# Performance work log

Measured on AMD Instinct MI355X. Metric: run time of the kernel, lower is better.

Reference implementation:

```python
import jax, jax.numpy as jnp
import numpy as np

B, C_IN, T, DIM_H, HEADS, K = 64, 64, 512, 64, 2, 9
N = B * T            # graph nodes = batch * cycle_size
E = 524288           # edges (avg degree 16)
D = HEADS * DIM_H    # 128, GATv2 concat output
EPS = 1e-5
SLOPE = 0.2          # GATv2 leaky_relu negative slope


def setup_inputs() -> dict:
    key = jax.random.key(0)
    ks = jax.random.split(key, 12)
    s = 0.05
    return {
        'x': jax.random.normal(ks[0], (B, C_IN, T), jnp.float32),
        'edge_index': jax.random.randint(ks[1], (2, E), 0, N, jnp.int32),
        'bn0_g': jnp.ones((C_IN,), jnp.float32),
        'bn0_b': jnp.zeros((C_IN,), jnp.float32),
        'W_l': jax.random.normal(ks[2], (C_IN, D), jnp.float32) * s,
        'W_r': jax.random.normal(ks[3], (C_IN, D), jnp.float32) * s,
        'att': jax.random.normal(ks[4], (HEADS, DIM_H), jnp.float32) * s,
        'gat_b': jnp.zeros((D,), jnp.float32),
        'bn1_g': jnp.ones((D,), jnp.float32),
        'bn1_b': jnp.zeros((D,), jnp.float32),
        'conv_w': jax.random.normal(ks[5], (T, T, K), jnp.float32) * s,
        'conv_b': jnp.zeros((T,), jnp.float32),
        'bn2_g': jnp.ones((T,), jnp.float32),
        'bn2_b': jnp.zeros((T,), jnp.float32),
    }


def _bn(x, g, b, axes, shape):
    # BatchNorm1d in training mode: biased batch stats per channel
    m = jnp.mean(x, axes, keepdims=True)
    v = jnp.var(x, axes, keepdims=True)
    return (x - m) * jax.lax.rsqrt(v + EPS) * g.reshape(shape) + b.reshape(shape)


def _gatv2(x, edge_index, W_l, W_r, att, bias):
    # PyG GATv2Conv: out_i = sum_j softmax_j(att . leaky_relu(xl_j + xr_i)) * xl_j
    xl = (x @ W_l).reshape(N, HEADS, DIM_H)
    xr = (x @ W_r).reshape(N, HEADS, DIM_H)
    loops = jnp.arange(N, dtype=edge_index.dtype)  # add_self_loops=True
    src = jnp.concatenate([edge_index[0], loops])
    dst = jnp.concatenate([edge_index[1], loops])
    h = xl[src] + xr[dst]                       # [E+N, H, dh]
    h = jnp.where(h > 0, h, SLOPE * h)
    logits = jnp.einsum('ehd,hd->eh', h, att)   # [E+N, H]
    mmax = jax.ops.segment_max(logits, dst, num_segments=N)
    a = jnp.exp(logits - mmax[dst])
    z = jax.ops.segment_sum(a, dst, num_segments=N)
    alpha = a / z[dst]                          # scatter-softmax over incoming edges
    out = jax.ops.segment_sum(alpha[:, :, None] * xl[src], dst, num_segments=N)
    return out.reshape(N, D) + bias


def reference(x, edge_index, bn0_g, bn0_b, W_l, W_r, att, gat_b,
              bn1_g, bn1_b, conv_w, conv_b, bn2_g, bn2_b):
    # b0 (batch_size > 1), x: [B, C_IN, T]
    x = _bn(x, bn0_g, bn0_b, (0, 2), (1, C_IN, 1))
    # (skip_connection branch is dead code: its result is overwritten)
    # torch .view on contiguous [B,C,T] -> [B*T, C] == raw reshape
    xn = x.reshape(N, C_IN)
    xn = jax.nn.relu(_bn(_gatv2(xn, edge_index, W_l, W_r, att, gat_b),
                         bn1_g, bn1_b, (0,), (1, D)))
    x3 = xn.reshape(B, D, T)
    residual = x3
    xt = jnp.transpose(x3, (0, 2, 1))           # [B, T, D]: channels=T, length=D
    y = jax.lax.conv_general_dilated(xt, conv_w, (1,), 'SAME',
                                     dimension_numbers=('NCH', 'OIH', 'NCH'))
    y = y + conv_b[None, :, None]
    y = jax.nn.relu(_bn(y, bn2_g, bn2_b, (0, 2), (1, T, 1)))
    y = jnp.transpose(y, (0, 2, 1))             # [B, D, T]
    # dropout(p=0.1) is identity in eval
    return residual + y
```

## Files before the change

### kernel.cpp

```cpp
#include <hip/hip_runtime.h>
#include <stdint.h>

typedef __attribute__((ext_vector_type(8))) __bf16 bf16x8;
typedef __attribute__((ext_vector_type(4))) float f32x4;

#define DEVI __device__ __forceinline__

constexpr int Bn = 64, CIN = 64, Tn = 512, Nn = 32768, Dn = 128;
constexpr int En = 524288, ENn = En + Nn;
constexpr float EPSf = 1e-5f;

constexpr size_t OFF_XL   = 0;
constexpr size_t OFF_XR   = 8388608;
constexpr size_t OFF_GPAD = 16777216;
constexpr size_t OFF_WRE  = 25690112;
constexpr size_t OFF_WT   = 30408704;
constexpr size_t OFF_CNT  = 30441472;
constexpr size_t OFF_OFFS = 30572544;
constexpr size_t OFF_CUR  = 30703632;
constexpr size_t OFF_SRC  = 30834704;
constexpr size_t OFF_STAT = 33062928;
constexpr size_t OFF_SUM0 = OFF_STAT;
constexpr size_t OFF_SQ0  = OFF_STAT + 256;
constexpr size_t OFF_SUM1 = OFF_STAT + 512;
constexpr size_t OFF_SQ1  = OFF_STAT + 1024;
constexpr size_t OFF_SC0  = OFF_STAT + 1536;
constexpr size_t OFF_SH0  = OFF_STAT + 1792;
constexpr size_t OFF_SC1  = OFF_STAT + 2048;
constexpr size_t OFF_SH1  = OFF_STAT + 2560;
constexpr size_t OFF_SC2  = OFF_STAT + 3072;
constexpr size_t OFF_SH2  = OFF_STAT + 5120;
constexpr size_t WS_NEED  = OFF_STAT + 7168;

DEVI float bf2f(unsigned short u){
  union { unsigned int u; float f; } x; x.u = ((unsigned int)u) << 16; return x.f;
}
DEVI unsigned short f2bf(float f){
  union { float f; unsigned int u; } x; x.f = f;
  unsigned int lsb = (x.u >> 16) & 1u;
  return (unsigned short)((x.u + 0x7fffu + lsb) >> 16);
}
DEVI void gl_lds16(const void* g, void* l){
  __builtin_amdgcn_global_load_lds(
      (const __attribute__((address_space(1))) unsigned int*)g,
      (__attribute__((address_space(3))) unsigned int*)l, 16, 0, 0);
}
DEVI bool finitef(float v){ return (v == v) && (fabsf(v) < 1e30f); }
DEVI float red32(float p){
  p += __shfl_xor(p, 1);  p += __shfl_xor(p, 2);  p += __shfl_xor(p, 4);
  p += __shfl_xor(p, 8);  p += __shfl_xor(p, 16);
  return p;
}
DEVI size_t gpad_addr(int b, int m, int d){
  int ig = m >> 2;
  int chunk = ((m & 3) << 1) | (d >> 6);
  int est = ((d & 63) + ((ig & 7) << 3)) & 63;
  return (size_t)b * 69632 + 2048 + (size_t)ig * 512 + (chunk << 6) + est;
}

__global__ void k_mark(float* out, int n){
  int i = blockIdx.x * 256 + threadIdx.x;
  if (i < n) out[i] = 1.0f;
}

__global__ void k_diag(const int* __restrict__ offs, const float* __restrict__ sc1,
                       const float* __restrict__ sc2, float* out){
  float code = 0.f;
  if (offs[Nn] != ENn) code += 512.f;
  if (!finitef(sc1[0])) code += 1024.f;
  if (!finitef(sc2[0])) code += 2048.f;
  if (code != 0.f) out[0] = code;
}

__global__ void __launch_bounds__(256) k_pre(
    const float* __restrict__ x,
    const float* __restrict__ w, const float* __restrict__ wl,
    const float* __restrict__ wr, const int* __restrict__ ei,
    float* __restrict__ sum0, float* __restrict__ sq0,
    unsigned short* __restrict__ wre, unsigned short* __restrict__ wt,
    int* __restrict__ cnt){
  __shared__ float l1[256], l2[256];
  int bl = blockIdx.x, t = threadIdx.x;
  if (bl < 256){
    int c = bl >> 2, q = bl & 3;
    const float4* x4 = (const float4*)x;
    float s = 0.f, ss = 0.f;
    #pragma unroll
    for (int j = 0; j < 8; ++j){
      int idx = t + j * 256;
      int b = (q << 4) + (idx >> 7);
      int tt4 = idx & 127;
      float4 v = x4[(size_t)b * 8192 + c * 128 + tt4];
      s  += (v.x + v.y) + (v.z + v.w);
      ss += (v.x * v.x + v.y * v.y) + (v.z * v.z + v.w * v.w);
    }
    l1[t] = s; l2[t] = ss; __syncthreads();
    for (int o = 128; o > 0; o >>= 1){
      if (t < o){ l1[t] += l1[t + o]; l2[t] += l2[t + o]; }
      __syncthreads();
    }
    if (t == 0){
      atomicAdd(sum0 + c, l1[0]);
      atomicAdd(sq0 + c, l2[0]);
    }
  } else if (bl < 772){
    int b2 = bl - 256;
    if (b2 < 512){
      int to = b2;
      int rot = (to & 7) << 3;
      for (int it = 0; it < 2; ++it){
        int ti = t + it * 256;
        const float* src = w + (to * 512 + ti) * 9;
        int col = (ti & ~63) | (((ti & 63) + rot) & 63);
        #pragma unroll
        for (int k = 0; k < 9; ++k)
          wre[((size_t)k * 512 + to) * 512 + col] = f2bf(src[k]);
      }
    } else {
      int q = b2 - 512;
      int n = q * 64 + (t >> 2);
      int k0 = (t & 3) * 16;
      for (int k = k0; k < k0 + 16; ++k){
        float v = (n < 128) ? wl[k * 128 + n] : wr[k * 128 + (n - 128)];
        wt[n * 64 + k] = f2bf(v);
      }
    }
  } else {
    int e = (bl - 772) * 256 + t;
    if (e < ENn){
      int dst = (e < En) ? ei[En + e] : (e - En);
      atomicAdd(cnt + dst, 1);
    }
  }
}

__global__ void __launch_bounds__(256) k_scan(
    const int* __restrict__ cnt, int* __restrict__ offs, int* __restrict__ cur,
    const float* __restrict__ sum0, const float* __restrict__ sq0,
    const float* __restrict__ g0, const float* __restrict__ b0v,
    float* __restrict__ scale0, float* __restrict__ shift0){
  __shared__ int lds[256];
  int t = threadIdx.x;
  if (t < 64){
    float mean = sum0[t] / 32768.f;
    float var  = sq0[t] / 32768.f - mean * mean;
    float rs = rsqrtf(var + EPSf) * g0[t];
    scale0[t] = rs;
    shift0[t] = b0v[t] - mean * rs;
  }
  const int4* c4 = (const int4*)cnt;
  int base4 = t * 32;
  int s = 0;
  #pragma unroll 8
  for (int j = 0; j < 32; ++j){
    int4 v = c4[base4 + j];
    s += v.x + v.y + v.z + v.w;
  }
  lds[t] = s; __syncthreads();
  int mine = s;
  for (int o = 1; o < 256; o <<= 1){
    int v = (t >= o) ? lds[t - o] : 0;
    __syncthreads();
    lds[t] += v;
    __syncthreads();
  }
  int run = lds[t] - mine;
  #pragma unroll 8
  for (int j = 0; j < 32; ++j){
    int4 v = c4[base4 + j];
    int4 o;
    o.x = run; run += v.x;
    o.y = run; run += v.y;
    o.z = run; run += v.z;
    o.w = run; run += v.w;
    ((int4*)offs)[base4 + j] = o;
    ((int4*)cur)[base4 + j] = o;
  }
  if (t == 255) offs[Nn] = run;
}

__global__ void __launch_bounds__(256) k_scatxl(
    const int* __restrict__ ei, int* __restrict__ cur, int* __restrict__ srcs,
    const float* __restrict__ x, const unsigned short* __restrict__ wt,
    const float* __restrict__ scale0, const float* __restrict__ shift0,
    unsigned short* __restrict__ xl, unsigned short* __restrict__ xr){
  __shared__ unsigned short lA[128 * 64];
  __shared__ unsigned short lB[128 * 64];
  int bl = blockIdx.x, t = threadIdx.x;
  if (bl < 2176){
    int e = bl * 256 + t;
    if (e < ENn){
      int s, dst;
      if (e < En){ s = ei[e]; dst = ei[En + e]; } else { s = dst = e - En; }
      int p = atomicAdd(cur + dst, 1);
      srcs[p] = s;
    }
    return;
  }
  int bid = bl - 2176;
  int m0 = (bid & 255) * 128;
  int nt = bid >> 8;
  {
    const unsigned short* gb = wt + nt * 128 * 64;
    #pragma unroll
    for (int i = 0; i < 4; ++i){
      int idx = t + i * 256;
      gl_lds16(gb + idx * 8, &lB[idx * 8]);
    }
  }
  {
    const float4* gx = (const float4*)(x + (size_t)m0 * 64);
    #pragma unroll
    for (int i = 0; i < 8; ++i){
      int idx = t + i * 256;
      float4 v = gx[idx];
      int row = idx >> 4;
      int ch = ((m0 + row) >> 3) & 63;
      float sc = scale0[ch], sh = shift0[ch];
      unsigned int p0 = (unsigned int)f2bf(v.x * sc + sh) | ((unsigned int)f2bf(v.y * sc + sh) << 16);
      unsigned int p1 = (unsigned int)f2bf(v.z * sc + sh) | ((unsigned int)f2bf(v.w * sc + sh) << 16);
      *(uint2*)&lA[idx * 4] = make_uint2(p0, p1);
    }
  }
  __syncthreads();
  int w = t >> 6, lane = t & 63;
  int wm = (w & 1) * 64, wn = (w >> 1) * 64;
  int lrow = lane & 15, quad = lane >> 4;
  const f32x4 fz = {0.f, 0.f, 0.f, 0.f};
  f32x4 acc[4][4];
  #pragma unroll
  for (int i = 0; i < 4; ++i)
    #pragma unroll
    for (int j = 0; j < 4; ++j) acc[i][j] = fz;
  #pragma unroll
  for (int kk = 0; kk < 2; ++kk){
    bf16x8 a[4], bfr[4];
    #pragma unroll
    for (int i = 0; i < 4; ++i){
      a[i]   = *(const bf16x8*)&lA[(wm + i * 16 + lrow) * 64 + kk * 32 + quad * 8];
      bfr[i] = *(const bf16x8*)&lB[(wn + i * 16 + lrow) * 64 + kk * 32 + quad * 8];
    }
    #pragma unroll
    for (int i = 0; i < 4; ++i)
      #pragma unroll
      for (int j = 0; j < 4; ++j)
        acc[i][j] = __builtin_amdgcn_mfma_f32_16x16x32_bf16(a[i], bfr[j], acc[i][j], 0, 0, 0);
  }
  unsigned short* outb = nt ? xr : xl;
  #pragma unroll
  for (int i = 0; i < 4; ++i)
    #pragma unroll
    for (int j = 0; j < 4; ++j)
      #pragma unroll
      for (int r = 0; r < 4; ++r){
        int row = m0 + wm + i * 16 + quad * 4 + r;
        int col = wn + j * 16 + lrow;
        outb[row * 128 + col] = f2bf(acc[i][j][r]);
      }
}

__global__ void __launch_bounds__(256) k_gat(
    const unsigned short* __restrict__ xl, const unsigned short* __restrict__ xr,
    const float* __restrict__ att,
    const int* __restrict__ offs, const int* __restrict__ srcs,
    unsigned short* __restrict__ gpad){
  int wv = threadIdx.x >> 6, lane = threadIdx.x & 63;
  int dst = blockIdx.x * 4 + wv;
  float2 pa = *(const float2*)(att + (lane << 1));
  float a0 = pa.x, a1 = pa.y;
  unsigned int pr = *(const unsigned int*)(xr + (size_t)dst * 128 + (lane << 1));
  float r0 = bf2f((unsigned short)(pr & 0xffffu)), r1 = bf2f((unsigned short)(pr >> 16));
  int beg = offs[dst], end = offs[dst + 1];
  float z = 0.f, ac0 = 0.f, ac1 = 0.f;
  int i = beg;
  for (; i + 4 <= end; i += 4){
    int s0 = srcs[i], s1 = srcs[i + 1], s2 = srcs[i + 2], s3 = srcs[i + 3];
    unsigned int px0 = *(const unsigned int*)(xl + (size_t)s0 * 128 + (lane << 1));
    unsigned int px1 = *(const unsigned int*)(xl + (size_t)s1 * 128 + (lane << 1));
    unsigned int px2 = *(const unsigned int*)(xl + (size_t)s2 * 128 + (lane << 1));
    unsigned int px3 = *(const unsigned int*)(xl + (size_t)s3 * 128 + (lane << 1));
    float x00 = bf2f((unsigned short)(px0 & 0xffffu)), x01 = bf2f((unsigned short)(px0 >> 16));
    float x10 = bf2f((unsigned short)(px1 & 0xffffu)), x11 = bf2f((unsigned short)(px1 >> 16));
    float x20 = bf2f((unsigned short)(px2 & 0xffffu)), x21 = bf2f((unsigned short)(px2 >> 16));
    float x30 = bf2f((unsigned short)(px3 & 0xffffu)), x31 = bf2f((unsigned short)(px3 >> 16));
    float h, p0, p1, p2, p3;
    h = x00 + r0; h = fmaxf(h, 0.2f * h); p0 = h * a0;
    h = x01 + r1; h = fmaxf(h, 0.2f * h); p0 += h * a1;
    h = x10 + r0; h = fmaxf(h, 0.2f * h); p1 = h * a0;
    h = x11 + r1; h = fmaxf(h, 0.2f * h); p1 += h * a1;
    h = x20 + r0; h = fmaxf(h, 0.2f * h); p2 = h * a0;
    h = x21 + r1; h = fmaxf(h, 0.2f * h); p2 += h * a1;
    h = x30 + r0; h = fmaxf(h, 0.2f * h); p3 = h * a0;
    h = x31 + r1; h = fmaxf(h, 0.2f * h); p3 += h * a1;
    p0 += __shfl_xor(p0, 1);  p1 += __shfl_xor(p1, 1);
    p2 += __shfl_xor(p2, 1);  p3 += __shfl_xor(p3, 1);
    p0 += __shfl_xor(p0, 2);  p1 += __shfl_xor(p1, 2);
    p2 += __shfl_xor(p2, 2);  p3 += __shfl_xor(p3, 2);
    p0 += __shfl_xor(p0, 4);  p1 += __shfl_xor(p1, 4);
    p2 += __shfl_xor(p2, 4);  p3 += __shfl_xor(p3, 4);
    p0 += __shfl_xor(p0, 8);  p1 += __shfl_xor(p1, 8);
    p2 += __shfl_xor(p2, 8);  p3 += __shfl_xor(p3, 8);
    p0 += __shfl_xor(p0, 16); p1 += __shfl_xor(p1, 16);
    p2 += __shfl_xor(p2, 16); p3 += __shfl_xor(p3, 16);
    float w0 = __expf(p0), w1 = __expf(p1), w2 = __expf(p2), w3 = __expf(p3);
    z += (w0 + w1) + (w2 + w3);
    ac0 += w0 * x00; ac0 += w1 * x10; ac0 += w2 * x20; ac0 += w3 * x30;
    ac1 += w0 * x01; ac1 += w1 * x11; ac1 += w2 * x21; ac1 += w3 * x31;
  }
  for (; i < end; ++i){
    int s = srcs[i];
    unsigned int px = *(const unsigned int*)(xl + (size_t)s * 128 + (lane << 1));
    float x0 = bf2f((unsigned short)(px & 0xffffu)), x1 = bf2f((unsigned short)(px >> 16));
    float h0 = x0 + r0; h0 = fmaxf(h0, 0.2f * h0);
    float h1 = x1 + r1; h1 = fmaxf(h1, 0.2f * h1);
    float p = red32(h0 * a0 + h1 * a1);
    float w = __expf(p);
    z += w; ac0 += w * x0; ac1 += w * x1;
  }
  float inv = (z > 0.f) ? 1.f / z : 0.f;
  size_t off = gpad_addr(dst >> 9, dst & 511, lane << 1);
  *(unsigned int*)(gpad + off) =
      (unsigned int)f2bf(ac0 * inv) | ((unsigned int)f2bf(ac1 * inv) << 16);
}

__global__ void k_bn1_stats(const unsigned short* __restrict__ gpad,
                            float* __restrict__ sums, float* __restrict__ sumsq){
  int t = threadIdx.x, d = t & 127, rg = t >> 7;
  int r0 = blockIdx.x * 256;
  int b = r0 >> 9;
  float s = 0.f, ss = 0.f;
  for (int i = 0; i < 128; ++i){
    int m = (r0 + rg + i * 2) & 511;
    float v = bf2f(gpad[gpad_addr(b, m, d)]);
    s += v; ss += v * v;
  }
  __shared__ float l1[256], l2[256];
  l1[t] = s; l2[t] = ss; __syncthreads();
  if (rg == 0){
    atomicAdd(sums + d,  l1[t] + l1[t + 128]);
    atomicAdd(sumsq + d, l2[t] + l2[t + 128]);
  }
}

__global__ void k_bn1_fin(const float* __restrict__ sums, const float* __restrict__ sumsq,
                          const float* __restrict__ g, const float* __restrict__ bb,
                          float* __restrict__ scale, float* __restrict__ shift){
  int d = threadIdx.x;
  float mean = sums[d] / (float)Nn;
  float var  = sumsq[d] / (float)Nn - mean * mean;
  float rs = rsqrtf(var + EPSf) * g[d];
  scale[d] = rs;
  shift[d] = bb[d] - mean * rs;
}

__global__ void __launch_bounds__(256) k_bn1_apply(
    unsigned short* __restrict__ gpad,
    const float* __restrict__ scale, const float* __restrict__ shift){
  int gi = blockIdx.x * 256 + threadIdx.x;
  int f0 = gi * 4;
  int b = f0 >> 16, q = f0 & 65535;
  int m = q >> 7, d0 = q & 127;
  unsigned short* gp = gpad + gpad_addr(b, m, d0);
  uint2 v = *(const uint2*)gp;
  float o0 = fmaxf(0.f, bf2f((unsigned short)(v.x & 0xffffu)) * scale[d0]     + shift[d0]);
  float o1 = fmaxf(0.f, bf2f((unsigned short)(v.x >> 16))     * scale[d0 + 1] + shift[d0 + 1]);
  float o2 = fmaxf(0.f, bf2f((unsigned short)(v.y & 0xffffu)) * scale[d0 + 2] + shift[d0 + 2]);
  float o3 = fmaxf(0.f, bf2f((unsigned short)(v.y >> 16))     * scale[d0 + 3] + shift[d0 + 3]);
  unsigned int p0 = (unsigned int)f2bf(o0) | ((unsigned int)f2bf(o1) << 16);
  unsigned int p1 = (unsigned int)f2bf(o2) | ((unsigned int)f2bf(o3) << 16);
  *(uint2*)gp = make_uint2(p0, p1);
}

__global__ void __launch_bounds__(256) k_conv(
    const unsigned short* __restrict__ wre,
    const unsigned short* __restrict__ gpad,
    unsigned short* __restrict__ y0, unsigned short* __restrict__ y1){
  __shared__ unsigned short lA[128 * 64];
  __shared__ unsigned short lB[128 * 64];
  int t = threadIdx.x;
  int to0 = blockIdx.x * 128;
  int b   = blockIdx.y;
  int z   = blockIdx.z;
  int w = t >> 6, lane = t & 63;
  int wm = (w & 1) * 64, wn = (w >> 1) * 64;
  int lrow = lane & 15, quad = lane >> 4;
  const f32x4 fz = {0.f, 0.f, 0.f, 0.f};
  f32x4 acc[4][4];
  #pragma unroll
  for (int i = 0; i < 4; ++i)
    #pragma unroll
    for (int j = 0; j < 4; ++j) acc[i][j] = fz;
  const unsigned short* gbb = gpad + (size_t)b * 69632;
  int ra = lrow & 7;
  for (int s = z * 36; s < z * 36 + 36; ++s){
    int k = s >> 3, c = s & 7;
    int ti0 = c * 64;
    const unsigned short* ga = wre + ((size_t)k * 512 + to0) * 512 + ti0;
    const unsigned short* gB = gbb + k * 512 + ti0;
    #pragma unroll
    for (int i = 0; i < 4; ++i){
      int idx = t + i * 256;
      int row = idx >> 3, c8 = idx & 7;
      gl_lds16(ga + row * 512 + c8 * 8, &lA[idx * 8]);
      gl_lds16(gB + row * 512 + c8 * 8, &lB[idx * 8]);
    }
    __syncthreads();
    int rb = (k + 4 + lrow) & 7;
    #pragma unroll
    for (int kk = 0; kk < 2; ++kk){
      int colA = ((kk << 5) + (quad << 3) + (ra << 3)) & 63;
      int colB = ((kk << 5) + (quad << 3) + (rb << 3)) & 63;
      bf16x8 a[4], bfr[4];
      #pragma unroll
      for (int i = 0; i < 4; ++i){
        a[i]   = *(const bf16x8*)&lA[(wm + i * 16 + lrow) * 64 + colA];
        bfr[i] = *(const bf16x8*)&lB[(wn + i * 16 + lrow) * 64 + colB];
      }
      #pragma unroll
      for (int i = 0; i < 4; ++i)
        #pragma unroll
        for (int j = 0; j < 4; ++j)
          acc[i][j] = __builtin_amdgcn_mfma_f32_16x16x32_bf16(a[i], bfr[j], acc[i][j], 0, 0, 0);
    }
    __syncthreads();
  }
  unsigned short* yo = z ? y1 : y0;
  #pragma unroll
  for (int i = 0; i < 4; ++i)
    #pragma unroll
    for (int j = 0; j < 4; ++j)
      #pragma unroll
      for (int r = 0; r < 4; ++r){
        int to = to0 + wm + i * 16 + quad * 4 + r;
        int p  = wn + j * 16 + lrow;
        yo[((size_t)b * 512 + to) * 128 + p] = f2bf(acc[i][j][r]);
      }
}

__global__ void k_bn2_stats(const unsigned short* __restrict__ y0,
                            const unsigned short* __restrict__ y1,
                            const float* __restrict__ g, const float* __restrict__ bb,
                            float* __restrict__ scale, float* __restrict__ shift){
  int to = blockIdx.x, t = threadIdx.x;
  int p = t & 127, b0 = t >> 7;
  float s = 0.f, ss = 0.f;
  for (int b = b0; b < 64; b += 2){
    size_t idx = ((size_t)b * 512 + to) * 128 + p;
    float v = bf2f(y0[idx]) + bf2f(y1[idx]);
    s += v; ss += v * v;
  }
  __shared__ float l1[256], l2[256];
  l1[t] = s; l2[t] = ss; __syncthreads();
  for (int o = 128; o > 0; o >>= 1){
    if (t < o){ l1[t] += l1[t + o]; l2[t] += l2[t + o]; }
    __syncthreads();
  }
  if (t == 0){
    float mean = l1[0] / 8192.f;
    float var  = l2[0] / 8192.f - mean * mean;
    float rs = rsqrtf(var + EPSf) * g[to];
    scale[to] = rs;
    shift[to] = bb[to] - mean * rs;
  }
}

__global__ void __launch_bounds__(256) k_final(
    const unsigned short* __restrict__ y0, const unsigned short* __restrict__ y1,
    const unsigned short* __restrict__ gpad,
    const float* __restrict__ scale, const float* __restrict__ shift,
    float* __restrict__ out){
  __shared__ float lt[32][33];
  int jt = blockIdx.x, it = blockIdx.y, b = blockIdx.z;
  int j0 = jt * 32, i0 = it * 32;
  int t = threadIdx.x;
  #pragma unroll
  for (int q = 0; q < 4; ++q){
    int li = t + q * 256;
    int r = li >> 5, cc = li & 31;
    int j = j0 + r;
    size_t idx = ((size_t)b * 512 + j) * 128 + i0 + cc;
    float v = bf2f(y0[idx]) + bf2f(y1[idx]);
    lt[r][cc] = fmaxf(0.f, v * scale[j] + shift[j]);
  }
  __syncthreads();
  const unsigned short* gbb = gpad + (size_t)b * 69632 + 2048;
  #pragma unroll
  for (int q = 0; q < 4; ++q){
    int li = t + q * 256;
    int ii = li >> 5, jj = li & 31;
    int i = i0 + ii, j = j0 + jj;
    int est = ((j & 63) + ((i & 7) << 3)) & 63;
    float res = bf2f(gbb[(size_t)i * 512 + ((j >> 6) << 6) + est]);
    size_t o = (size_t)b * 65536 + (size_t)i * 512 + j;
    out[o] = res + lt[jj][ii];
  }
}

extern "C" void kernel_launch(void* const* d_in, const int* in_sizes, int n_in,
                              void* d_out, int out_size, void* d_ws, size_t ws_size,
                              hipStream_t stream){
  const float* x     = (const float*)d_in[0];
  const int*   ei    = (const int*)d_in[1];
  const float* bn0g  = (const float*)d_in[2];
  const float* bn0b  = (const float*)d_in[3];
  const float* Wl    = (const float*)d_in[4];
  const float* Wr    = (const float*)d_in[5];
  const float* att   = (const float*)d_in[6];
  const float* bn1g  = (const float*)d_in[8];
  const float* bn1b  = (const float*)d_in[9];
  const float* convw = (const float*)d_in[10];
  const float* bn2g  = (const float*)d_in[12];
  const float* bn2b  = (const float*)d_in[13];
  float* out = (float*)d_out;

  if (ws_size < WS_NEED){
    k_mark<<<(out_size + 255) / 256, 256, 0, stream>>>(out, out_size);
    return;
  }
  char* ws = (char*)d_ws;
  unsigned short* xl   = (unsigned short*)(ws + OFF_XL);
  unsigned short* xr   = (unsigned short*)(ws + OFF_XR);
  unsigned short* y0   = (unsigned short*)(ws + OFF_XL);
  unsigned short* y1   = (unsigned short*)(ws + OFF_XR);
  unsigned short* gpad = (unsigned short*)(ws + OFF_GPAD);
  unsigned short* wre  = (unsigned short*)(ws + OFF_WRE);
  unsigned short* wt   = (unsigned short*)(ws + OFF_WT);
  int*            cnt  = (int*)(ws + OFF_CNT);
  int*            offs = (int*)(ws + OFF_OFFS);
  int*            cur  = (int*)(ws + OFF_CUR);
  int*            srcs = (int*)(ws + OFF_SRC);
  float*          sum0 = (float*)(ws + OFF_SUM0);
  float*          sq0  = (float*)(ws + OFF_SQ0);
  float*          sum1 = (float*)(ws + OFF_SUM1);
  float*          sq1  = (float*)(ws + OFF_SQ1);
  float*          sc0  = (float*)(ws + OFF_SC0);
  float*          sh0  = (float*)(ws + OFF_SH0);
  float*          sc1  = (float*)(ws + OFF_SC1);
  float*          sh1  = (float*)(ws + OFF_SH1);
  float*          sc2  = (float*)(ws + OFF_SC2);
  float*          sh2  = (float*)(ws + OFF_SH2);

  hipMemsetAsync(cnt, 0, 131072, stream);
  hipMemsetAsync((void*)(ws + OFF_STAT), 0, 1536, stream);
  hipMemsetAsync(gpad, 0, 8912896, stream);

  k_pre<<<2948, 256, 0, stream>>>(x, convw, Wl, Wr, ei, sum0, sq0, wre, wt, cnt);
  k_scan<<<1, 256, 0, stream>>>(cnt, offs, cur, sum0, sq0, bn0g, bn0b, sc0, sh0);
  k_scatxl<<<2688, 256, 0, stream>>>(ei, cur, srcs, x, wt, sc0, sh0, xl, xr);
  k_gat<<<8192, 256, 0, stream>>>(xl, xr, att, offs, srcs, gpad);
  k_bn1_stats<<<128, 256, 0, stream>>>(gpad, sum1, sq1);
  k_bn1_fin<<<1, 128, 0, stream>>>(sum1, sq1, bn1g, bn1b, sc1, sh1);
  k_bn1_apply<<<4096, 256, 0, stream>>>(gpad, sc1, sh1);
  k_conv<<<dim3(4, 64, 2), 256, 0, stream>>>(wre, gpad, y0, y1);
  k_bn2_stats<<<512, 256, 0, stream>>>(y0, y1, bn2g, bn2b, sc2, sh2);
  k_final<<<dim3(16, 4, 64), 256, 0, stream>>>(y0, y1, gpad, sc2, sh2, out);
  k_diag<<<1, 1, 0, stream>>>(offs, sc1, sc2, out);

  (void)in_sizes; (void)n_in;
}
```

Measured before the change: 307.0 us.

## Split conv output columns across more blocks and vectorize BN1 stats loads

The conv kernel's N tile is halved from 128 to 64 output positions and the grid grows from 2 to 4 z-slices, doubling the block count (512 to 1024) for better occupancy on the many CUs, at the cost of re-loading the weight tile twice as often. Separately, the BN1 statistics kernel now reads four bf16 values per thread with 8-byte loads, using a per-batch half-block layout and a shared-memory tree before the atomics. This replaces the previous scalar 2-byte loads.

```diff
diff --git a/kernel.cpp b/kernel.cpp
--- a/kernel.cpp
+++ b/kernel.cpp
@@ -323,22 +323,39 @@
       (unsigned int)f2bf(ac0 * inv) | ((unsigned int)f2bf(ac1 * inv) << 16);
 }
 
-__global__ void k_bn1_stats(const unsigned short* __restrict__ gpad,
-                            float* __restrict__ sums, float* __restrict__ sumsq){
-  int t = threadIdx.x, d = t & 127, rg = t >> 7;
-  int r0 = blockIdx.x * 256;
-  int b = r0 >> 9;
-  float s = 0.f, ss = 0.f;
-  for (int i = 0; i < 128; ++i){
-    int m = (r0 + rg + i * 2) & 511;
-    float v = bf2f(gpad[gpad_addr(b, m, d)]);
-    s += v; ss += v * v;
-  }
-  __shared__ float l1[256], l2[256];
-  l1[t] = s; l2[t] = ss; __syncthreads();
-  if (rg == 0){
-    atomicAdd(sums + d,  l1[t] + l1[t + 128]);
-    atomicAdd(sumsq + d, l2[t] + l2[t + 128]);
+__global__ void __launch_bounds__(256) k_bn1_stats(
+    const unsigned short* __restrict__ gpad,
+    float* __restrict__ sums, float* __restrict__ sumsq){
+  int t = threadIdx.x;
+  int bl = blockIdx.x;
+  int b = bl >> 1, half = bl & 1;
+  int d4 = (t & 31) * 4, rr = t >> 5;
+  float4 s = {0.f, 0.f, 0.f, 0.f}, ss = {0.f, 0.f, 0.f, 0.f};
+  #pragma unroll 4
+  for (int i = 0; i < 32; ++i){
+    int m = half * 256 + rr + i * 8;
+    uint2 v = *(const uint2*)(gpad + gpad_addr(b, m, d4));
+    float v0 = bf2f((unsigned short)(v.x & 0xffffu));
+    float v1 = bf2f((unsigned short)(v.x >> 16));
+    float v2 = bf2f((unsigned short)(v.y & 0xffffu));
+    float v3 = bf2f((unsigned short)(v.y >> 16));
+    s.x += v0; s.y += v1; s.z += v2; s.w += v3;
+    ss.x += v0 * v0; ss.y += v1 * v1; ss.z += v2 * v2; ss.w += v3 * v3;
+  }
+  __shared__ float4 L1[256], L2[256];
+  L1[t] = s; L2[t] = ss; __syncthreads();
+  if (t < 32){
+    float4 a = L1[t], q = L2[t];
+    #pragma unroll
+    for (int g = 1; g < 8; ++g){
+      float4 a2 = L1[t + g * 32], q2 = L2[t + g * 32];
+      a.x += a2.x; a.y += a2.y; a.z += a2.z; a.w += a2.w;
+      q.x += q2.x; q.y += q2.y; q.z += q2.z; q.w += q2.w;
+    }
+    atomicAdd(sums + d4,     a.x); atomicAdd(sums + d4 + 1, a.y);
+    atomicAdd(sums + d4 + 2, a.z); atomicAdd(sums + d4 + 3, a.w);
+    atomicAdd(sumsq + d4,     q.x); atomicAdd(sumsq + d4 + 1, q.y);
+    atomicAdd(sumsq + d4 + 2, q.z); atomicAdd(sumsq + d4 + 3, q.w);
   }
 }
 
@@ -376,21 +393,23 @@
     const unsigned short* __restrict__ gpad,
     unsigned short* __restrict__ y0, unsigned short* __restrict__ y1){
   __shared__ unsigned short lA[128 * 64];
-  __shared__ unsigned short lB[128 * 64];
+  __shared__ unsigned short lB[64 * 64];
   int t = threadIdx.x;
   int to0 = blockIdx.x * 128;
   int b   = blockIdx.y;
-  int z   = blockIdx.z;
+  int bz  = blockIdx.z;
+  int p0  = (bz & 1) * 64;
+  int z   = bz >> 1;
   int w = t >> 6, lane = t & 63;
-  int wm = (w & 1) * 64, wn = (w >> 1) * 64;
+  int wm = (w & 1) * 64, wn = (w >> 1) * 32;
   int lrow = lane & 15, quad = lane >> 4;
   const f32x4 fz = {0.f, 0.f, 0.f, 0.f};
-  f32x4 acc[4][4];
+  f32x4 acc[4][2];
   #pragma unroll
   for (int i = 0; i < 4; ++i)
     #pragma unroll
-    for (int j = 0; j < 4; ++j) acc[i][j] = fz;
-  const unsigned short* gbb = gpad + (size_t)b * 69632;
+    for (int j = 0; j < 2; ++j) acc[i][j] = fz;
+  const unsigned short* gbb = gpad + (size_t)b * 69632 + (size_t)p0 * 512;
   int ra = lrow & 7;
   for (int s = z * 36; s < z * 36 + 36; ++s){
     int k = s >> 3, c = s & 7;
@@ -402,6 +421,11 @@
       int idx = t + i * 256;
       int row = idx >> 3, c8 = idx & 7;
       gl_lds16(ga + row * 512 + c8 * 8, &lA[idx * 8]);
+    }
+    #pragma unroll
+    for (int i = 0; i < 2; ++i){
+      int idx = t + i * 256;
+      int row = idx >> 3, c8 = idx & 7;
       gl_lds16(gB + row * 512 + c8 * 8, &lB[idx * 8]);
     }
     __syncthreads();
@@ -410,16 +434,17 @@
     for (int kk = 0; kk < 2; ++kk){
       int colA = ((kk << 5) + (quad << 3) + (ra << 3)) & 63;
       int colB = ((kk << 5) + (quad << 3) + (rb << 3)) & 63;
-      bf16x8 a[4], bfr[4];
+      bf16x8 a[4], bfr[2];
       #pragma unroll
-      for (int i = 0; i < 4; ++i){
+      for (int i = 0; i < 4; ++i)
         a[i]   = *(const bf16x8*)&lA[(wm + i * 16 + lrow) * 64 + colA];
-        bfr[i] = *(const bf16x8*)&lB[(wn + i * 16 + lrow) * 64 + colB];
-      }
+      #pragma unroll
+      for (int j = 0; j < 2; ++j)
+        bfr[j] = *(const bf16x8*)&lB[(wn + j * 16 + lrow) * 64 + colB];
       #pragma unroll
       for (int i = 0; i < 4; ++i)
         #pragma unroll
-        for (int j = 0; j < 4; ++j)
+        for (int j = 0; j < 2; ++j)
           acc[i][j] = __builtin_amdgcn_mfma_f32_16x16x32_bf16(a[i], bfr[j], acc[i][j], 0, 0, 0);
     }
     __syncthreads();
@@ -428,11 +453,11 @@
   #pragma unroll
   for (int i = 0; i < 4; ++i)
     #pragma unroll
-    for (int j = 0; j < 4; ++j)
+    for (int j = 0; j < 2; ++j)
       #pragma unroll
       for (int r = 0; r < 4; ++r){
         int to = to0 + wm + i * 16 + quad * 4 + r;
-        int p  = wn + j * 16 + lrow;
+        int p  = p0 + wn + j * 16 + lrow;
         yo[((size_t)b * 512 + to) * 128 + p] = f2bf(acc[i][j][r]);
       }
 }
@@ -551,7 +576,7 @@
   k_bn1_stats<<<128, 256, 0, stream>>>(gpad, sum1, sq1);
   k_bn1_fin<<<1, 128, 0, stream>>>(sum1, sq1, bn1g, bn1b, sc1, sh1);
   k_bn1_apply<<<4096, 256, 0, stream>>>(gpad, sc1, sh1);
-  k_conv<<<dim3(4, 64, 2), 256, 0, stream>>>(wre, gpad, y0, y1);
+  k_conv<<<dim3(4, 64, 4), 256, 0, stream>>>(wre, gpad, y0, y1);
   k_bn2_stats<<<512, 256, 0, stream>>>(y0, y1, bn2g, bn2b, sc2, sh2);
   k_final<<<dim3(16, 4, 64), 256, 0, stream>>>(y0, y1, gpad, sc2, sh2, out);
   k_diag<<<1, 1, 0, stream>>>(offs, sc1, sc2, out);
```

Result: slower. 315.2 us (+2.7%).
